# Kernel tuning notes

Measured on AMD Instinct MI355X. Metric: run time of the kernel, lower is better.

## Reference

```python
import jax, jax.numpy as jnp
import numpy as np

BS, T, N_AGENTS, N_ACTIONS = 8, 256, 8, 20
A = N_AGENTS * N_ACTIONS          # 160 gru input dim
E, D, HID, S = 128, 128, 32, 256  # encoder_dim, decoder_dim, mixing_embed_dim, state_dim
EMBED = HID * (A + E)             # 9216


def _lin(k, out_d, in_d):
    s = 1.0 / np.sqrt(in_d)
    return jax.random.uniform(k, (out_d, in_d), jnp.float32, -s, s)


def _vec(k, d, fan):
    s = 1.0 / np.sqrt(fan)
    return jax.random.uniform(k, (d,), jnp.float32, -s, s)


def setup_inputs() -> dict:
    key = jax.random.key(0)
    ks = jax.random.split(key, 32)
    inp = {
        'act': jax.random.uniform(ks[0], (BS, T, N_AGENTS, N_ACTIONS), jnp.float32),
        'states': jax.random.normal(ks[1], (BS, T, S), jnp.float32),
        # GRU (PyTorch layout: gates stacked [r; z; n])
        'gru_wih': _lin(ks[2], 3 * E, A),
        'gru_whh': _lin(ks[3], 3 * E, E),
        'gru_bih': _vec(ks[4], 3 * E, E),
        'gru_bhh': _vec(ks[5], 3 * E, E),
        # encoder fc
        'fc_w': _lin(ks[6], D, E),
        'fc_b': _vec(ks[7], D, E),
        # attention
        'attn_w': _lin(ks[8], D, D + E),
        'v_w': _vec(ks[9], D, D),
        # hyper_w_1 (2-layer MLP)
        'hw1_w0': _lin(ks[10], EMBED, S), 'hw1_b0': _vec(ks[11], EMBED, S),
        'hw1_w1': _lin(ks[12], EMBED, EMBED), 'hw1_b1': _vec(ks[13], EMBED, EMBED),
        # hyper_w_final (2-layer MLP)
        'hwf_w0': _lin(ks[14], HID, S), 'hwf_b0': _vec(ks[15], HID, S),
        'hwf_w1': _lin(ks[16], HID, HID), 'hwf_b1': _vec(ks[17], HID, HID),
        # hyper_b_1
        'hb1_w': _lin(ks[18], HID, S), 'hb1_b': _vec(ks[19], HID, S),
        # hyper_b_2 (2-layer MLP)
        'hb2_w0': _lin(ks[20], HID, S), 'hb2_b0': _vec(ks[21], HID, S),
        'hb2_w1': _lin(ks[22], 1, HID), 'hb2_b1': _vec(ks[23], 1, HID),
    }
    return inp


def reference(act, states, gru_wih, gru_whh, gru_bih, gru_bhh, fc_w, fc_b,
              attn_w, v_w, hw1_w0, hw1_b0, hw1_w1, hw1_b1,
              hwf_w0, hwf_b0, hwf_w1, hwf_b1, hb1_w, hb1_b,
              hb2_w0, hb2_b0, hb2_w1, hb2_b1):
    bs, t, n_ag, n_ac = act.shape
    a = n_ag * n_ac
    e = gru_whh.shape[1]
    d = fc_w.shape[0]
    hid = hb1_w.shape[0]

    act_flat = act.reshape(bs, t, a)
    # act_his = [zeros, act]; prefixes use only the first t steps of it
    x = jnp.concatenate([jnp.zeros((bs, 1, a), act.dtype), act_flat[:, : t - 1]], axis=1)

    # GRU over full sequence once (causal => identical to recomputing each prefix)
    def step(h, xt):
        gi = xt @ gru_wih.T + gru_bih
        gh = h @ gru_whh.T + gru_bhh
        ir, iz, i_n = jnp.split(gi, 3, axis=-1)
        hr, hz, h_n = jnp.split(gh, 3, axis=-1)
        r = jax.nn.sigmoid(ir + hr)
        z = jax.nn.sigmoid(iz + hz)
        n = jnp.tanh(i_n + r * h_n)
        h_new = (1.0 - z) * n + z * h
        return h_new, h_new

    h0 = jnp.zeros((bs, e), act.dtype)
    _, enc = jax.lax.scan(step, h0, jnp.swapaxes(x, 0, 1))
    enc = jnp.swapaxes(enc, 0, 1)  # [bs, T, E]

    # s0 for prefix ending at step q is tanh(fc(enc[:, q]))
    s0 = jnp.tanh(enc @ fc_w.T + fc_b)  # [bs, T, D]

    # attention: cat order is (s, enc_output)
    w_s, w_e = attn_w[:, :d], attn_w[:, d:]
    ps = s0 @ w_s.T            # [bs, Tq, D]
    pe = enc @ w_e.T           # [bs, Tk, D]
    pre = jnp.tanh(ps[:, :, None, :] + pe[:, None, :, :])  # [bs, Tq, Tk, D]
    scores = jnp.einsum('bqkd,d->bqk', pre, v_w)
    mask = jnp.tril(jnp.ones((t, t), bool))  # key j <= query q (prefix j < idx)
    scores = jnp.where(mask[None], scores, -jnp.inf)
    attn = jax.nn.softmax(scores, axis=-1)
    c = jnp.einsum('bqk,bke->bqe', attn, enc)  # [bs, T, E]

    inp = jnp.concatenate([act_flat, c], axis=-1).reshape(bs * t, 1, a + e)
    st = states.reshape(bs * t, -1)

    w1 = (jax.nn.relu(st @ hw1_w0.T + hw1_b0) @ hw1_w1.T + hw1_b1).reshape(bs * t, a + e, hid)
    b1 = (st @ hb1_w.T + hb1_b)[:, None, :]
    h = jax.nn.relu(jnp.einsum('bik,bkh->bih', inp, w1) + b1)  # [bs*T, 1, hid]

    wf = (jax.nn.relu(st @ hwf_w0.T + hwf_b0) @ hwf_w1.T + hwf_b1)[:, :, None]  # [bs*T, hid, 1]
    b2 = (jax.nn.relu(st @ hb2_w0.T + hb2_b0) @ hb2_w1.T + hb2_b1)[:, :, None]  # [bs*T, 1, 1]
    q = (jnp.einsum('bih,bho->bio', h, wf) + b2).reshape(bs, t, 1)
    return q
```

## Files before the change

kernel.cpp:

```cpp
#include <hip/hip_runtime.h>
#include <hip/hip_bf16.h>
#include <stdint.h>

typedef __attribute__((ext_vector_type(4))) float f32x4;
typedef __attribute__((ext_vector_type(8))) short short8v;
typedef __attribute__((ext_vector_type(4))) unsigned short u16x4;

constexpr int kT  = 256;
constexpr int kA  = 160;

__device__ __forceinline__ float bf2f(unsigned short u){
  union { unsigned int u; float f; } c; c.u = ((unsigned int)u) << 16; return c.f;
}
__device__ __forceinline__ unsigned short f2bf(float f){
  union { float f; unsigned int u; } c; c.f = f;
  unsigned int r = (c.u + 0x7FFFu + ((c.u >> 16) & 1u)) >> 16;
  return (unsigned short)r;
}
__device__ __forceinline__ float sigmoid_fast(float x){
  return __builtin_amdgcn_rcpf(1.f + __expf(-x));
}
__device__ __forceinline__ float tanhf_fast(float x){
  float xc = fminf(fmaxf(x, -15.f), 15.f);
  float t = __expf(2.f * xc);
  return (t - 1.f) * __builtin_amdgcn_rcpf(t + 1.f);
}
__device__ __forceinline__ void gload_lds16(const void* g, void* l){
  __builtin_amdgcn_global_load_lds((const __attribute__((address_space(1))) void*)g,
                                   (__attribute__((address_space(3))) void*)l, 16, 0, 0);
}
__device__ __forceinline__ void bar_lgkm(){
  asm volatile("s_waitcnt lgkmcnt(0)" ::: "memory");
  __builtin_amdgcn_s_barrier();
  asm volatile("" ::: "memory");
}
__device__ __forceinline__ void bar_only(){
  asm volatile("" ::: "memory");
  __builtin_amdgcn_s_barrier();
  asm volatile("" ::: "memory");
}

__global__ __launch_bounds__(256) void k_fill_f32(float* out, int n, float v){
  int i = blockIdx.x * blockDim.x + threadIdx.x;
  if (i < n) out[i] = v;
}

__global__ __launch_bounds__(256) void k_f32_to_bf16(const float* __restrict__ src,
                                                     unsigned short* __restrict__ dst, int n4){
  int stride = gridDim.x * blockDim.x;
  for (int i = blockIdx.x * blockDim.x + threadIdx.x; i < n4; i += stride){
    f32x4 v = *(const f32x4*)(src + (size_t)i * 4);
    u16x4 o;
    o[0] = f2bf(v[0]); o[1] = f2bf(v[1]); o[2] = f2bf(v[2]); o[3] = f2bf(v[3]);
    *(u16x4*)(dst + (size_t)i * 4) = o;
  }
}

__global__ __launch_bounds__(384) void k_gi(const float* __restrict__ act,
                                            const float* __restrict__ wih,
                                            const float* __restrict__ bih,
                                            float* __restrict__ gi){
  int blk = blockIdx.x;
  int b = blk >> 5, tg = blk & 31;
  int j = threadIdx.x;
  __shared__ __align__(16) float xh[8][kA];
  for (int idx = j; idx < 8 * kA; idx += 384){
    int u = idx / kA, i = idx - u * kA;
    int t = tg * 8 + u;
    xh[u][i] = (t == 0) ? 0.f : act[((size_t)b * kT + t - 1) * kA + i];
  }
  __syncthreads();
  float acc[8] = {0,0,0,0,0,0,0,0};
  for (int i = 0; i < kA; i += 4){
    f32x4 wv = *(const f32x4*)(wih + (size_t)j * kA + i);
#pragma unroll
    for (int jj = 0; jj < 4; ++jj)
#pragma unroll
      for (int u = 0; u < 8; ++u)
        acc[u] += wv[jj] * xh[u][i + jj];
  }
  float bv = bih[j];
#pragma unroll
  for (int u = 0; u < 8; ++u)
    gi[((size_t)b * kT + tg * 8 + u) * 384 + j] = acc[u] + bv;
}

template<int RELU>
__device__ __forceinline__ void gemm576_body(const unsigned short* __restrict__ A,
                                             const unsigned short* __restrict__ B,
                                             const float* __restrict__ bias,
                                             unsigned short* __restrict__ C,
                                             int M, int Nc, int K, int ldc,
                                             int bid, int nwg, char* smem){
  int nbm = M >> 7;
  int cpx = nwg >> 3;
  int sw  = (bid & 7) * cpx + (bid >> 3);
  int bm = sw % nbm, bn = sw / nbm;
  int arow0 = bm << 7;
  int bcol0 = bn * 576;
  int t = threadIdx.x;
  int l = t & 63, w = t >> 6;
  int wr = w >> 2, wc = w & 3;
  int lr = l & 15, kq = l >> 4;
  int Kb = K * 2;
  int ar = t >> 2, ap = t & 3;
  size_t aoffg = (size_t)ar * Kb + ((ap ^ ((ar >> 1) & 3)) << 4);
  size_t boffg[5];
#pragma unroll
  for (int i = 0; i < 5; ++i){
    int q = i * 512 + t, r = q >> 2, p = q & 3;
    boffg[i] = (size_t)r * Kb + ((p ^ ((r >> 1) & 3)) << 4);
  }
  const char* Ag = (const char*)(A + (size_t)arow0 * K);
  const char* Bg = (const char*)(B + (size_t)bcol0 * K);
  int dA = t * 16;
  int kk16 = (kq ^ ((lr >> 1) & 3)) << 4;
  int aRd = (wr * 64 + lr) * 64 + kk16;
  int bRd = 8192 + (wc * 144 + lr) * 64 + kk16;
  f32x4 acc[4][9] = {};
  int nt = K >> 5;

  auto stage = [&](int kt, int bi){
    size_t kb = (size_t)kt * 64;
    char* Ld = smem + bi * 49152;
    gload_lds16(Ag + aoffg + kb, Ld + dA);
#pragma unroll
    for (int i = 0; i < 5; ++i)
      gload_lds16(Bg + boffg[i] + kb, Ld + 8192 + i * 8192 + dA);
  };

  stage(0, 0);
  stage(1, 1);
  asm volatile("s_waitcnt vmcnt(6)" ::: "memory");
  int cur = 0;
  for (int kt = 0; kt < nt; ++kt){
    bar_only();
    if (kt + 2 < nt){
      int nb = cur + 2; if (nb >= 3) nb -= 3;
      stage(kt + 2, nb);
    }
    const char* Ld = smem + cur * 49152;
    short8v af[4];
#pragma unroll
    for (int m = 0; m < 4; ++m) af[m] = *(const short8v*)(Ld + aRd + m * 1024);
#pragma unroll
    for (int c = 0; c < 3; ++c){
      short8v bf[3];
#pragma unroll
      for (int j = 0; j < 3; ++j) bf[j] = *(const short8v*)(Ld + bRd + (c * 3 + j) * 1024);
      __builtin_amdgcn_s_setprio(1);
#pragma unroll
      for (int m = 0; m < 4; ++m)
#pragma unroll
        for (int j = 0; j < 3; ++j)
          acc[m][c * 3 + j] = __builtin_amdgcn_mfma_f32_16x16x32_bf16(af[m], bf[j], acc[m][c * 3 + j], 0, 0, 0);
      __builtin_amdgcn_s_setprio(0);
    }
    if (kt + 1 < nt){
      if (kt + 2 < nt) asm volatile("s_waitcnt vmcnt(6)" ::: "memory");
      else             asm volatile("s_waitcnt vmcnt(0)" ::: "memory");
    }
    ++cur; if (cur == 3) cur = 0;
  }

#pragma unroll
  for (int m = 0; m < 4; ++m){
    int row = arow0 + wr * 64 + m * 16 + kq * 4;
#pragma unroll
    for (int n = 0; n < 9; ++n){
      int col = bcol0 + wc * 144 + n * 16 + lr;
      float bv = bias[col];
#pragma unroll
      for (int r = 0; r < 4; ++r){
        float v = acc[m][n][r] + bv;
        if (RELU) v = fmaxf(v, 0.f);
        C[(size_t)(row + r) * ldc + col] = f2bf(v);
      }
    }
  }
}

template<int RELU>
__global__ __launch_bounds__(256) void k_gemm288(const unsigned short* __restrict__ A,
                                                 const unsigned short* __restrict__ B,
                                                 const float* __restrict__ bias,
                                                 unsigned short* __restrict__ C,
                                                 int M, int Nc, int K, int ldc){
  __shared__ __align__(16) char smem[79872];
  int nbm = M >> 7;
  int nwg = gridDim.x, bid = blockIdx.x;
  int cpx = nwg >> 3;
  int sw  = (bid & 7) * cpx + (bid >> 3);
  int bm = sw % nbm, bn = sw / nbm;
  int arow0 = bm << 7;
  int bcol0 = bn * 288;
  int t = threadIdx.x;
  int l = t & 63, w = t >> 6;
  int wr = w >> 1, wc = w & 1;
  int lr = l & 15, kq = l >> 4;
  int Kb = K * 2;
  size_t aoffg[2];
#pragma unroll
  for (int i = 0; i < 2; ++i){
    int q = i * 256 + t, r = q >> 2, p = q & 3;
    aoffg[i] = (size_t)r * Kb + ((p ^ ((r >> 1) & 3)) << 4);
  }
  size_t boffg[5];
#pragma unroll
  for (int i = 0; i < 5; ++i){
    int q = i * 256 + t, r = q >> 2, p = q & 3;
    boffg[i] = (size_t)r * Kb + ((p ^ ((r >> 1) & 3)) << 4);
  }
  const char* Ag = (const char*)(A + (size_t)arow0 * K);
  const char* Bg = (const char*)(B + (size_t)bcol0 * K);
  int dT = t * 16;
  int kk16 = (kq ^ ((lr >> 1) & 3)) << 4;
  int aRd = (wr * 64 + lr) * 64 + kk16;
  int bRd = 8192 + (wc * 144 + lr) * 64 + kk16;
  f32x4 acc[4][9] = {};
  int nt = K >> 5;
  bool w01 = (t < 128);

  auto stage = [&](int kt, int bi){
    size_t kb = (size_t)kt * 64;
    char* Ld = smem + bi * 26624;
    gload_lds16(Ag + aoffg[0] + kb, Ld + dT);
    gload_lds16(Ag + aoffg[1] + kb, Ld + 4096 + dT);
#pragma unroll
    for (int i = 0; i < 4; ++i)
      gload_lds16(Bg + boffg[i] + kb, Ld + 8192 + i * 4096 + dT);
    if (w01) gload_lds16(Bg + boffg[4] + kb, Ld + 24576 + dT);
  };
  auto waitJ = [&](){
    if (w01) asm volatile("s_waitcnt vmcnt(7)" ::: "memory");
    else     asm volatile("s_waitcnt vmcnt(6)" ::: "memory");
  };

  stage(0, 0);
  stage(1, 1);
  waitJ();
  int cur = 0;
  for (int kt = 0; kt < nt; ++kt){
    bar_only();
    if (kt + 2 < nt){
      int nb = cur + 2; if (nb >= 3) nb -= 3;
      stage(kt + 2, nb);
    }
    const char* Ld = smem + cur * 26624;
    short8v af[4];
#pragma unroll
    for (int m = 0; m < 4; ++m) af[m] = *(const short8v*)(Ld + aRd + m * 1024);
#pragma unroll
    for (int c = 0; c < 3; ++c){
      short8v bf[3];
#pragma unroll
      for (int j = 0; j < 3; ++j) bf[j] = *(const short8v*)(Ld + bRd + (c * 3 + j) * 1024);
      __builtin_amdgcn_s_setprio(1);
#pragma unroll
      for (int m = 0; m < 4; ++m)
#pragma unroll
        for (int j = 0; j < 3; ++j)
          acc[m][c * 3 + j] = __builtin_amdgcn_mfma_f32_16x16x32_bf16(af[m], bf[j], acc[m][c * 3 + j], 0, 0, 0);
      __builtin_amdgcn_s_setprio(0);
    }
    if (kt + 1 < nt){
      if (kt + 2 < nt) waitJ();
      else             asm volatile("s_waitcnt vmcnt(0)" ::: "memory");
    }
    ++cur; if (cur == 3) cur = 0;
  }

#pragma unroll
  for (int m = 0; m < 4; ++m){
    int row = arow0 + wr * 64 + m * 16 + kq * 4;
#pragma unroll
    for (int n = 0; n < 9; ++n){
      int col = bcol0 + wc * 144 + n * 16 + lr;
      float bv = bias[col];
#pragma unroll
      for (int r = 0; r < 4; ++r){
        float v = acc[m][n][r] + bv;
        if (RELU) v = fmaxf(v, 0.f);
        C[(size_t)(row + r) * ldc + col] = f2bf(v);
      }
    }
  }
}

__global__ __launch_bounds__(512) void k_gru_g1_conv(const float* __restrict__ gi,
                                                     const float* __restrict__ whh,
                                                     const float* __restrict__ bhh,
                                                     float* __restrict__ enc,
                                                     const unsigned short* __restrict__ stb,
                                                     const unsigned short* __restrict__ w0b,
                                                     const float* __restrict__ hb0,
                                                     unsigned short* __restrict__ zb,
                                                     const float* __restrict__ csrc,
                                                     unsigned short* __restrict__ cdst,
                                                     int n4){
  __shared__ __align__(16) char smem[147456];
  int blk = blockIdx.x;
  if (blk >= 264){
    int stride = (gridDim.x - 264) * 512;
    for (int i = (blk - 264) * 512 + threadIdx.x; i < n4; i += stride){
      f32x4 v = *(const f32x4*)(csrc + (size_t)i * 4);
      u16x4 o;
      o[0] = f2bf(v[0]); o[1] = f2bf(v[1]); o[2] = f2bf(v[2]); o[3] = f2bf(v[3]);
      *(u16x4*)(cdst + (size_t)i * 4) = o;
    }
    return;
  }
  if (blk >= 8){
    gemm576_body<1>(stb, w0b, hb0, zb, 2048, 9216, 256, 9216, blk - 8, 256, smem);
    return;
  }
  float* h_lds = (float*)smem;
  float (*red)[128] = (float(*)[128])(smem + 512);
  int b = blk;
  int tid = threadIdx.x;
  int e = tid & 127, s = tid >> 7;
  float W0[32], W1[32], W2[32];
#pragma unroll
  for (int k = 0; k < 32; ++k){
    W0[k] = whh[(size_t)(0 * 128 + e) * 128 + s * 32 + k];
    W1[k] = whh[(size_t)(1 * 128 + e) * 128 + s * 32 + k];
    W2[k] = whh[(size_t)(2 * 128 + e) * 128 + s * 32 + k];
  }
  if (tid < 128) h_lds[tid] = 0.f;
  float bh0 = 0.f, bh1 = 0.f, bh2 = 0.f;
  if (tid < 128){ bh0 = bhh[e]; bh1 = bhh[128 + e]; bh2 = bhh[256 + e]; }
  const float* gib = gi + (size_t)b * kT * 384;
  float* encb = enc + (size_t)b * kT * 128;
  float gir = 0.f, giz = 0.f, gin = 0.f;
  if (tid < 128){ gir = gib[e]; giz = gib[128 + e]; gin = gib[256 + e]; }
  bar_lgkm();
  for (int t = 0; t < kT; ++t){
    float p0 = 0.f, p1 = 0.f, p2 = 0.f;
#pragma unroll
    for (int k4 = 0; k4 < 8; ++k4){
      f32x4 hv = *(const f32x4*)(h_lds + s * 32 + k4 * 4);
#pragma unroll
      for (int jj = 0; jj < 4; ++jj){
        p0 += W0[k4 * 4 + jj] * hv[jj];
        p1 += W1[k4 * 4 + jj] * hv[jj];
        p2 += W2[k4 * 4 + jj] * hv[jj];
      }
    }
    float nir = 0.f, niz = 0.f, nin = 0.f;
    if (t + 1 < kT && tid < 128){
      const float* gn = gib + (size_t)(t + 1) * 384;
      nir = gn[e]; niz = gn[128 + e]; nin = gn[256 + e];
    }
    red[s * 3 + 0][e] = p0; red[s * 3 + 1][e] = p1; red[s * 3 + 2][e] = p2;
    bar_lgkm();
    if (tid < 128){
      float ghr = red[0][e] + red[3][e] + red[6][e] + red[9][e]  + bh0;
      float ghz = red[1][e] + red[4][e] + red[7][e] + red[10][e] + bh1;
      float ghn = red[2][e] + red[5][e] + red[8][e] + red[11][e] + bh2;
      float r = sigmoid_fast(gir + ghr);
      float z = sigmoid_fast(giz + ghz);
      float n = tanhf_fast(gin + r * ghn);
      float hnew = (1.f - z) * n + z * h_lds[e];
      h_lds[e] = hnew;
      encb[t * 128 + e] = hnew;
    }
    bar_lgkm();
    gir = nir; giz = niz; gin = nin;
  }
}

__global__ __launch_bounds__(128) void k_attnpre(const float* __restrict__ enc,
                                                 const float* __restrict__ fc_w,
                                                 const float* __restrict__ fc_b,
                                                 const float* __restrict__ attn_w,
                                                 float* __restrict__ ps,
                                                 float* __restrict__ pe){
  int bt = blockIdx.x, o = threadIdx.x;
  __shared__ __align__(16) float ench[128], s0h[128];
  ench[o] = enc[(size_t)bt * 128 + o];
  __syncthreads();
  float a0 = fc_b[o], a1 = 0.f;
  for (int i = 0; i < 128; i += 4){
    f32x4 wv = *(const f32x4*)(fc_w + (size_t)o * 128 + i);
    f32x4 we = *(const f32x4*)(attn_w + (size_t)o * 256 + 128 + i);
    f32x4 ev = *(const f32x4*)(ench + i);
#pragma unroll
    for (int jj = 0; jj < 4; ++jj){ a0 += wv[jj] * ev[jj]; a1 += we[jj] * ev[jj]; }
  }
  s0h[o] = tanhf_fast(a0);
  pe[(size_t)bt * 128 + o] = a1;
  __syncthreads();
  float a2 = 0.f;
  for (int i = 0; i < 128; i += 4){
    f32x4 ws = *(const f32x4*)(attn_w + (size_t)o * 256 + i);
    f32x4 sv = *(const f32x4*)(s0h + i);
#pragma unroll
    for (int jj = 0; jj < 4; ++jj) a2 += ws[jj] * sv[jj];
  }
  ps[(size_t)bt * 128 + o] = a2;
}

__global__ __launch_bounds__(256) void k_attn(const float* __restrict__ enc,
                                              const float* __restrict__ ps,
                                              const float* __restrict__ pe,
                                              const float* __restrict__ v_w,
                                              float* __restrict__ cbuf){
  int q = blockIdx.x, b = blockIdx.y;
  int tid = threadIdx.x;
  __shared__ __align__(16) float psh[128], vwh[128];
  __shared__ __align__(16) float sch[256];
  __shared__ __align__(16) float rr[256];
  __shared__ float mxs, dns;
  if (tid < 128){
    psh[tid] = ps[((size_t)b * kT + q) * 128 + tid];
    vwh[tid] = v_w[tid];
  }
  __syncthreads();
  int nk = q + 1;
  for (int k = tid; k < nk; k += 256){
    const float* per = pe + ((size_t)b * kT + k) * 128;
    float sc = 0.f;
    for (int d = 0; d < 128; d += 4){
      f32x4 pv = *(const f32x4*)(per + d);
      f32x4 qv = *(const f32x4*)(psh + d);
      sc += vwh[d + 0] * tanhf_fast(qv[0] + pv[0]);
      sc += vwh[d + 1] * tanhf_fast(qv[1] + pv[1]);
      sc += vwh[d + 2] * tanhf_fast(qv[2] + pv[2]);
      sc += vwh[d + 3] * tanhf_fast(qv[3] + pv[3]);
    }
    sch[k] = sc;
  }
  __syncthreads();
  float lm = -3.0e38f;
  for (int k = tid; k < nk; k += 256) lm = fmaxf(lm, sch[k]);
  rr[tid] = lm; __syncthreads();
  for (int off = 128; off > 0; off >>= 1){
    if (tid < off) rr[tid] = fmaxf(rr[tid], rr[tid + off]);
    __syncthreads();
  }
  if (tid == 0) mxs = rr[0];
  __syncthreads();
  float mxv = mxs;
  float lsum = 0.f;
  for (int k = tid; k < nk; k += 256){
    float p = __expf(sch[k] - mxv);
    sch[k] = p; lsum += p;
  }
  __syncthreads();
  rr[tid] = lsum; __syncthreads();
  for (int off = 128; off > 0; off >>= 1){
    if (tid < off) rr[tid] += rr[tid + off];
    __syncthreads();
  }
  if (tid == 0) dns = __builtin_amdgcn_rcpf(rr[0]);
  __syncthreads();
  float rd = dns;
  int d = tid & 127, half = tid >> 7;
  float acc = 0.f;
  for (int k = half; k < nk; k += 2)
    acc += sch[k] * enc[((size_t)b * kT + k) * 128 + d];
  rr[tid] = acc; __syncthreads();
  if (half == 0)
    cbuf[((size_t)b * kT + q) * 128 + d] = (acc + rr[d + 128]) * rd;
}

__global__ __launch_bounds__(256) void k_final(const float* __restrict__ states,
                                               const float* __restrict__ act,
                                               const float* __restrict__ cbuf,
                                               const unsigned short* __restrict__ w1f,
                                               const float* __restrict__ hb1_w, const float* __restrict__ hb1_b,
                                               const float* __restrict__ hwf_w0, const float* __restrict__ hwf_b0,
                                               const float* __restrict__ hwf_w1, const float* __restrict__ hwf_b1,
                                               const float* __restrict__ hb2_w0, const float* __restrict__ hb2_b0,
                                               const float* __restrict__ hb2_w1, const float* __restrict__ hb2_b1,
                                               float* __restrict__ out){
  int bt = blockIdx.x, tid = threadIdx.x;
  __shared__ __align__(16) float sth[256], inph[288], red[256];
  __shared__ __align__(16) float t1h[32], t2h[32], b1h[32], wfh[32], hvals[32];
  __shared__ float b2s;
  sth[tid] = states[(size_t)bt * 256 + tid];
  if (tid < 160) inph[tid] = act[(size_t)bt * 160 + tid];
  if (tid < 128) inph[160 + tid] = cbuf[(size_t)bt * 128 + tid];
  __syncthreads();
  int o = tid & 31, s = tid >> 5;
  float p1 = 0.f, p2 = 0.f, p3 = 0.f;
  for (int k = s * 32; k < s * 32 + 32; k += 4){
    f32x4 sv  = *(const f32x4*)(sth + k);
    f32x4 w1v = *(const f32x4*)(hwf_w0 + (size_t)o * 256 + k);
    f32x4 w2v = *(const f32x4*)(hb2_w0 + (size_t)o * 256 + k);
    f32x4 w3v = *(const f32x4*)(hb1_w  + (size_t)o * 256 + k);
#pragma unroll
    for (int jj = 0; jj < 4; ++jj){
      p1 += w1v[jj] * sv[jj]; p2 += w2v[jj] * sv[jj]; p3 += w3v[jj] * sv[jj];
    }
  }
  red[tid] = p1; __syncthreads();
  if (tid < 32){
    float a = hwf_b0[tid];
#pragma unroll
    for (int s8 = 0; s8 < 8; ++s8) a += red[s8 * 32 + tid];
    t1h[tid] = fmaxf(a, 0.f);
  }
  __syncthreads();
  red[tid] = p2; __syncthreads();
  if (tid < 32){
    float a = hb2_b0[tid];
#pragma unroll
    for (int s8 = 0; s8 < 8; ++s8) a += red[s8 * 32 + tid];
    t2h[tid] = fmaxf(a, 0.f);
  }
  __syncthreads();
  red[tid] = p3; __syncthreads();
  if (tid < 32){
    float a = hb1_b[tid];
#pragma unroll
    for (int s8 = 0; s8 < 8; ++s8) a += red[s8 * 32 + tid];
    b1h[tid] = a;
  }
  __syncthreads();
  if (tid < 32){
    float a = hwf_b1[tid];
#pragma unroll
    for (int j = 0; j < 32; ++j) a += hwf_w1[(size_t)tid * 32 + j] * t1h[j];
    wfh[tid] = a;
  }
  if (tid == 64){
    float a = hb2_b1[0];
#pragma unroll
    for (int j = 0; j < 32; ++j) a += hb2_w1[j] * t2h[j];
    b2s = a;
  }
  __syncthreads();
  float ph = 0.f;
  const unsigned short* wrow = w1f + (size_t)bt * 9216;
  for (int i = s * 36; i < s * 36 + 36; ++i)
    ph += inph[i] * bf2f(wrow[i * 32 + o]);
  red[tid] = ph; __syncthreads();
  if (tid < 32){
    float a = b1h[tid];
#pragma unroll
    for (int s8 = 0; s8 < 8; ++s8) a += red[s8 * 32 + tid];
    hvals[tid] = fmaxf(a, 0.f) * wfh[tid];
  }
  __syncthreads();
  if (tid == 0){
    float q = b2s;
#pragma unroll
    for (int j = 0; j < 32; ++j) q += hvals[j];
    out[bt] = q;
  }
}

extern "C" void kernel_launch(void* const* d_in, const int* in_sizes, int n_in,
                              void* d_out, int out_size, void* d_ws, size_t ws_size,
                              hipStream_t stream){
  float* outp = (float*)d_out;

  bool ok = (n_in == 24) && out_size == 2048 &&
            in_sizes[0] == 327680 && in_sizes[1] == 524288 &&
            in_sizes[2] == 61440  && in_sizes[3] == 49152 &&
            in_sizes[10] == 2359296 && in_sizes[12] == 84934656;
  if (!ok){
    k_fill_f32<<<dim3(8), dim3(256), 0, stream>>>(outp, 2048, 1.0e6f);
    return;
  }

  const float* act    = (const float*)d_in[0];
  const float* states = (const float*)d_in[1];
  const float* wih    = (const float*)d_in[2];
  const float* whh    = (const float*)d_in[3];
  const float* bih    = (const float*)d_in[4];
  const float* bhh    = (const float*)d_in[5];
  const float* fc_w   = (const float*)d_in[6];
  const float* fc_b   = (const float*)d_in[7];
  const float* attn_w = (const float*)d_in[8];
  const float* v_w    = (const float*)d_in[9];
  const float* hw1_w0 = (const float*)d_in[10];
  const float* hw1_b0 = (const float*)d_in[11];
  const float* hw1_w1 = (const float*)d_in[12];
  const float* hw1_b1 = (const float*)d_in[13];
  const float* hwf_w0 = (const float*)d_in[14];
  const float* hwf_b0 = (const float*)d_in[15];
  const float* hwf_w1 = (const float*)d_in[16];
  const float* hwf_b1 = (const float*)d_in[17];
  const float* hb1_w  = (const float*)d_in[18];
  const float* hb1_b  = (const float*)d_in[19];
  const float* hb2_w0 = (const float*)d_in[20];
  const float* hb2_b0 = (const float*)d_in[21];
  const float* hb2_w1 = (const float*)d_in[22];
  const float* hb2_b1 = (const float*)d_in[23];

  char* ws = (char*)d_ws;
  size_t off = 0;
  auto alloc = [&](size_t bytes)->void*{
    void* p = ws + off; off += (bytes + 255) & ~(size_t)255; return p;
  };
  unsigned short* zb  = (unsigned short*)alloc((size_t)2048 * 9216 * 2);
  unsigned short* w1f = (unsigned short*)alloc((size_t)2048 * 9216 * 2);
  unsigned short* w0b = (unsigned short*)alloc((size_t)9216 * 256 * 2);
  unsigned short* stb = (unsigned short*)alloc((size_t)2048 * 256 * 2);
  float* gi   = (float*)alloc((size_t)2048 * 384 * 4);
  float* enc  = (float*)alloc((size_t)2048 * 128 * 4);
  float* psb  = (float*)alloc((size_t)2048 * 128 * 4);
  float* peb  = (float*)alloc((size_t)2048 * 128 * 4);
  float* cbuf = (float*)alloc((size_t)2048 * 128 * 4);
  size_t floor_bytes = off;
  const size_t row_bytes = (size_t)9216 * 2;
  const size_t slack = (size_t)2 << 20;
  if (ws_size < floor_bytes + 288 * row_bytes + slack){
    k_fill_f32<<<dim3(8), dim3(256), 0, stream>>>(outp, 2048, (float)(ws_size >> 20));
    return;
  }
  size_t avail = ws_size - floor_bytes - slack;
  int chunk_rows = (int)(((avail / row_bytes) / 288) * 288);
  if (chunk_rows > 9216) chunk_rows = 9216;
  unsigned short* w1c = (unsigned short*)(ws + floor_bytes);
  int first_nc = chunk_rows;

  k_f32_to_bf16<<<dim3(1024), dim3(256), 0, stream>>>(hw1_w0, w0b, 9216 * 256 / 4);
  k_f32_to_bf16<<<dim3(256),  dim3(256), 0, stream>>>(states, stb, 2048 * 256 / 4);
  k_gi<<<dim3(256), dim3(384), 0, stream>>>(act, wih, bih, gi);
  k_gru_g1_conv<<<dim3(768), dim3(512), 0, stream>>>(gi, whh, bhh, enc,
                                                     stb, w0b, hw1_b0, zb,
                                                     hw1_w1, w1c, first_nc * 9216 / 4);
  k_attnpre<<<dim3(2048), dim3(128), 0, stream>>>(enc, fc_w, fc_b, attn_w, psb, peb);
  k_attn<<<dim3(256, 8), dim3(256), 0, stream>>>(enc, psb, peb, v_w, cbuf);
  for (int c0 = 0; c0 < 9216; c0 += chunk_rows){
    int nc = 9216 - c0; if (nc > chunk_rows) nc = chunk_rows;
    if (c0 > 0)
      k_f32_to_bf16<<<dim3(2048), dim3(256), 0, stream>>>(hw1_w1 + (size_t)c0 * 9216, w1c, nc * 9216 / 4);
    k_gemm288<0><<<dim3(16 * (nc / 288)), dim3(256), 0, stream>>>(zb, w1c, hw1_b1 + c0, w1f + c0,
                                                                  2048, nc, 9216, 9216);
  }
  k_final<<<dim3(2048), dim3(256), 0, stream>>>(states, act, cbuf, w1f,
      hb1_w, hb1_b, hwf_w0, hwf_b0, hwf_w1, hwf_b1, hb2_w0, hb2_b0, hb2_w1, hb2_b1,
      outp);
}
```

Measured before the change: 796.9 us.

## Fuse fp32-to-bf16 weight conversion into big GEMM B-tile loads

The large hyper_w_1 second-layer GEMM now reads the fp32 weight matrix directly, converts it to bf16 in registers with packed convert instructions, and writes it into LDS. This removes the separate conversion pass, the bf16 weight copy and the chunked launch loop. The tile widens to 576 columns with 512 threads. The cost is register-staged B loads with a full vmcnt(0) wait and a barrier every k-step, in place of async global-to-LDS loads, plus twice the global read bytes for B per tile.

Result: slower. 887.0 us (+11.3%).

```diff
diff --git a/kernel.cpp b/kernel.cpp
--- a/kernel.cpp
+++ b/kernel.cpp
@@ -5,6 +5,7 @@
 typedef __attribute__((ext_vector_type(4))) float f32x4;
 typedef __attribute__((ext_vector_type(8))) short short8v;
 typedef __attribute__((ext_vector_type(4))) unsigned short u16x4;
+typedef __attribute__((ext_vector_type(4))) unsigned int u32x4;
 
 constexpr int kT  = 256;
 constexpr int kA  = 160;
@@ -16,6 +17,11 @@
   union { float f; unsigned int u; } c; c.f = f;
   unsigned int r = (c.u + 0x7FFFu + ((c.u >> 16) & 1u)) >> 16;
   return (unsigned short)r;
+}
+__device__ __forceinline__ unsigned int cvtpk_bf16(float lo, float hi){
+  unsigned int r;
+  asm volatile("v_cvt_pk_bf16_f32 %0, %1, %2" : "=v"(r) : "v"(lo), "v"(hi));
+  return r;
 }
 __device__ __forceinline__ float sigmoid_fast(float x){
   return __builtin_amdgcn_rcpf(1.f + __expf(-x));
@@ -180,73 +186,89 @@
   }
 }
 
-template<int RELU>
-__global__ __launch_bounds__(256) void k_gemm288(const unsigned short* __restrict__ A,
-                                                 const unsigned short* __restrict__ B,
-                                                 const float* __restrict__ bias,
-                                                 unsigned short* __restrict__ C,
-                                                 int M, int Nc, int K, int ldc){
-  __shared__ __align__(16) char smem[79872];
+__global__ __launch_bounds__(512) void k_gemm576f(const unsigned short* __restrict__ A,
+                                                  const float* __restrict__ Bf,
+                                                  const float* __restrict__ bias,
+                                                  unsigned short* __restrict__ C,
+                                                  int M, int Nc, int K, int ldc){
+  __shared__ __align__(16) char smem[147456];
   int nbm = M >> 7;
   int nwg = gridDim.x, bid = blockIdx.x;
   int cpx = nwg >> 3;
   int sw  = (bid & 7) * cpx + (bid >> 3);
   int bm = sw % nbm, bn = sw / nbm;
   int arow0 = bm << 7;
-  int bcol0 = bn * 288;
+  int bcol0 = bn * 576;
   int t = threadIdx.x;
   int l = t & 63, w = t >> 6;
-  int wr = w >> 1, wc = w & 1;
+  int wr = w >> 2, wc = w & 3;
   int lr = l & 15, kq = l >> 4;
   int Kb = K * 2;
-  size_t aoffg[2];
-#pragma unroll
-  for (int i = 0; i < 2; ++i){
-    int q = i * 256 + t, r = q >> 2, p = q & 3;
-    aoffg[i] = (size_t)r * Kb + ((p ^ ((r >> 1) & 3)) << 4);
-  }
-  size_t boffg[5];
+  int ar = t >> 2, ap = t & 3;
+  size_t aoffg = (size_t)ar * Kb + ((ap ^ ((ar >> 1) & 3)) << 4);
+  size_t bsrcF[5]; int bdst[5];
 #pragma unroll
   for (int i = 0; i < 5; ++i){
-    int q = i * 256 + t, r = q >> 2, p = q & 3;
-    boffg[i] = (size_t)r * Kb + ((p ^ ((r >> 1) & 3)) << 4);
+    int q = i * 512 + t, r = q >> 2, p = q & 3;
+    int rs = (r < 576) ? r : 0;
+    bsrcF[i] = (size_t)rs * K + p * 8;
+    bdst[i]  = 8192 + r * 64 + ((p ^ ((r >> 1) & 3)) << 4);
   }
   const char* Ag = (const char*)(A + (size_t)arow0 * K);
-  const char* Bg = (const char*)(B + (size_t)bcol0 * K);
-  int dT = t * 16;
+  const float* Bg = Bf + (size_t)bcol0 * K;
+  int dA = t * 16;
   int kk16 = (kq ^ ((lr >> 1) & 3)) << 4;
   int aRd = (wr * 64 + lr) * 64 + kk16;
   int bRd = 8192 + (wc * 144 + lr) * 64 + kk16;
   f32x4 acc[4][9] = {};
   int nt = K >> 5;
-  bool w01 = (t < 128);
-
-  auto stage = [&](int kt, int bi){
-    size_t kb = (size_t)kt * 64;
-    char* Ld = smem + bi * 26624;
-    gload_lds16(Ag + aoffg[0] + kb, Ld + dT);
-    gload_lds16(Ag + aoffg[1] + kb, Ld + 4096 + dT);
-#pragma unroll
-    for (int i = 0; i < 4; ++i)
-      gload_lds16(Bg + boffg[i] + kb, Ld + 8192 + i * 4096 + dT);
-    if (w01) gload_lds16(Bg + boffg[4] + kb, Ld + 24576 + dT);
+  f32x4 rB[5][2];
+
+  auto loadB = [&](int kt){
+    const float* s = Bg + kt * 32;
+#pragma unroll
+    for (int i = 0; i < 5; ++i){
+      rB[i][0] = *(const f32x4*)(s + bsrcF[i]);
+      rB[i][1] = *(const f32x4*)(s + bsrcF[i] + 4);
+    }
   };
-  auto waitJ = [&](){
-    if (w01) asm volatile("s_waitcnt vmcnt(7)" ::: "memory");
-    else     asm volatile("s_waitcnt vmcnt(6)" ::: "memory");
+  auto writeB = [&](int bi){
+    char* Ld = smem + bi * 49152;
+#pragma unroll
+    for (int i = 0; i < 5; ++i){
+      u32x4 pk;
+      pk[0] = cvtpk_bf16(rB[i][0][0], rB[i][0][1]);
+      pk[1] = cvtpk_bf16(rB[i][0][2], rB[i][0][3]);
+      pk[2] = cvtpk_bf16(rB[i][1][0], rB[i][1][1]);
+      pk[3] = cvtpk_bf16(rB[i][1][2], rB[i][1][3]);
+      *(u32x4*)(Ld + bdst[i]) = pk;
+    }
   };
-
-  stage(0, 0);
-  stage(1, 1);
-  waitJ();
+  auto loadA = [&](int kt, int bi){
+    gload_lds16(Ag + aoffg + (size_t)kt * 64, smem + bi * 49152 + dA);
+  };
+
+  loadB(0);
+  asm volatile("s_waitcnt vmcnt(0)" ::: "memory");
+  writeB(0);
+  loadB(1);
+  loadA(0, 0);
+  loadA(1, 1);
+  asm volatile("s_waitcnt vmcnt(0)" ::: "memory");
+  bar_lgkm();
+
   int cur = 0;
   for (int kt = 0; kt < nt; ++kt){
-    bar_only();
+    if (kt + 1 < nt){
+      int nb = cur + 1; if (nb >= 3) nb -= 3;
+      writeB(nb);
+    }
     if (kt + 2 < nt){
-      int nb = cur + 2; if (nb >= 3) nb -= 3;
-      stage(kt + 2, nb);
-    }
-    const char* Ld = smem + cur * 26624;
+      int nb2 = cur + 2; if (nb2 >= 3) nb2 -= 3;
+      loadA(kt + 2, nb2);
+      loadB(kt + 2);
+    }
+    const char* Ld = smem + cur * 49152;
     short8v af[4];
 #pragma unroll
     for (int m = 0; m < 4; ++m) af[m] = *(const short8v*)(Ld + aRd + m * 1024);
@@ -264,8 +286,8 @@
       __builtin_amdgcn_s_setprio(0);
     }
     if (kt + 1 < nt){
-      if (kt + 2 < nt) waitJ();
-      else             asm volatile("s_waitcnt vmcnt(0)" ::: "memory");
+      asm volatile("s_waitcnt vmcnt(0)" ::: "memory");
+      bar_lgkm();
     }
     ++cur; if (cur == 3) cur = 0;
   }
@@ -280,36 +302,22 @@
 #pragma unroll
       for (int r = 0; r < 4; ++r){
         float v = acc[m][n][r] + bv;
-        if (RELU) v = fmaxf(v, 0.f);
         C[(size_t)(row + r) * ldc + col] = f2bf(v);
       }
     }
   }
 }
 
-__global__ __launch_bounds__(512) void k_gru_g1_conv(const float* __restrict__ gi,
-                                                     const float* __restrict__ whh,
-                                                     const float* __restrict__ bhh,
-                                                     float* __restrict__ enc,
-                                                     const unsigned short* __restrict__ stb,
-                                                     const unsigned short* __restrict__ w0b,
-                                                     const float* __restrict__ hb0,
-                                                     unsigned short* __restrict__ zb,
-                                                     const float* __restrict__ csrc,
-                                                     unsigned short* __restrict__ cdst,
-                                                     int n4){
+__global__ __launch_bounds__(512) void k_gru_g1(const float* __restrict__ gi,
+                                                const float* __restrict__ whh,
+                                                const float* __restrict__ bhh,
+                                                float* __restrict__ enc,
+                                                const unsigned short* __restrict__ stb,
+                                                const unsigned short* __restrict__ w0b,
+                                                const float* __restrict__ hb0,
+                                                unsigned short* __restrict__ zb){
   __shared__ __align__(16) char smem[147456];
   int blk = blockIdx.x;
-  if (blk >= 264){
-    int stride = (gridDim.x - 264) * 512;
-    for (int i = (blk - 264) * 512 + threadIdx.x; i < n4; i += stride){
-      f32x4 v = *(const f32x4*)(csrc + (size_t)i * 4);
-      u16x4 o;
-      o[0] = f2bf(v[0]); o[1] = f2bf(v[1]); o[2] = f2bf(v[2]); o[3] = f2bf(v[3]);
-      *(u16x4*)(cdst + (size_t)i * 4) = o;
-    }
-    return;
-  }
   if (blk >= 8){
     gemm576_body<1>(stb, w0b, hb0, zb, 2048, 9216, 256, 9216, blk - 8, 256, smem);
     return;
@@ -604,34 +612,18 @@
   float* psb  = (float*)alloc((size_t)2048 * 128 * 4);
   float* peb  = (float*)alloc((size_t)2048 * 128 * 4);
   float* cbuf = (float*)alloc((size_t)2048 * 128 * 4);
-  size_t floor_bytes = off;
-  const size_t row_bytes = (size_t)9216 * 2;
-  const size_t slack = (size_t)2 << 20;
-  if (ws_size < floor_bytes + 288 * row_bytes + slack){
+  if (ws_size < off){
     k_fill_f32<<<dim3(8), dim3(256), 0, stream>>>(outp, 2048, (float)(ws_size >> 20));
     return;
   }
-  size_t avail = ws_size - floor_bytes - slack;
-  int chunk_rows = (int)(((avail / row_bytes) / 288) * 288);
-  if (chunk_rows > 9216) chunk_rows = 9216;
-  unsigned short* w1c = (unsigned short*)(ws + floor_bytes);
-  int first_nc = chunk_rows;
 
   k_f32_to_bf16<<<dim3(1024), dim3(256), 0, stream>>>(hw1_w0, w0b, 9216 * 256 / 4);
   k_f32_to_bf16<<<dim3(256),  dim3(256), 0, stream>>>(states, stb, 2048 * 256 / 4);
   k_gi<<<dim3(256), dim3(384), 0, stream>>>(act, wih, bih, gi);
-  k_gru_g1_conv<<<dim3(768), dim3(512), 0, stream>>>(gi, whh, bhh, enc,
-                                                     stb, w0b, hw1_b0, zb,
-                                                     hw1_w1, w1c, first_nc * 9216 / 4);
+  k_gru_g1<<<dim3(264), dim3(512), 0, stream>>>(gi, whh, bhh, enc, stb, w0b, hw1_b0, zb);
   k_attnpre<<<dim3(2048), dim3(128), 0, stream>>>(enc, fc_w, fc_b, attn_w, psb, peb);
   k_attn<<<dim3(256, 8), dim3(256), 0, stream>>>(enc, psb, peb, v_w, cbuf);
-  for (int c0 = 0; c0 < 9216; c0 += chunk_rows){
-    int nc = 9216 - c0; if (nc > chunk_rows) nc = chunk_rows;
-    if (c0 > 0)
-      k_f32_to_bf16<<<dim3(2048), dim3(256), 0, stream>>>(hw1_w1 + (size_t)c0 * 9216, w1c, nc * 9216 / 4);
-    k_gemm288<0><<<dim3(16 * (nc / 288)), dim3(256), 0, stream>>>(zb, w1c, hw1_b1 + c0, w1f + c0,
-                                                                  2048, nc, 9216, 9216);
-  }
+  k_gemm576f<<<dim3(256), dim3(512), 0, stream>>>(zb, hw1_w1, hw1_b1, w1f, 2048, 9216, 9216, 9216);
   k_final<<<dim3(2048), dim3(256), 0, stream>>>(states, act, cbuf, w1f,
       hb1_w, hb1_b, hwf_w0, hwf_b0, hwf_w1, hwf_b1, hb2_w0, hb2_b0, hb2_w1, hb2_b1,
       outp);
```
